# Kernel optimization log

Measured on AMD Instinct MI355X. Metric: run time of the kernel, lower is better.

## Reference

```python
import jax, jax.numpy as jnp
import numpy as np

# Winograd F(4x4, 3x3) transform matrices (wincnn convention, as in jiecaoyu/winograd)
BT = jnp.array([
    [4.,  0., -5.,  0., 1., 0.],
    [0., -4., -4.,  1., 1., 0.],
    [0.,  4., -4., -1., 1., 0.],
    [0., -2., -1.,  2., 1., 0.],
    [0.,  2., -1., -2., 1., 0.],
    [0.,  4.,  0., -5., 0., 1.]], dtype=jnp.float32)  # [6,6]
AT = jnp.array([
    [1., 1.,  1., 1.,  1., 0.],
    [0., 1., -1., 2., -2., 0.],
    [0., 1.,  1., 4.,  4., 0.],
    [0., 1., -1., 8., -8., 1.]], dtype=jnp.float32)  # [4,6]

KERNEL = 3
PAD = 1
GROUPS = 1
TILE_IN = 6   # input_tile_size
TILE_OUT = 4  # output_tile_size


def setup_inputs() -> dict:
    key = jax.random.key(0)
    k1, k2, k3 = jax.random.split(key, 3)
    N, Cin, H, W = 16, 64, 128, 128
    Cout = 64
    x = jax.random.normal(k1, (N, Cin, H, W), dtype=jnp.float32)
    # weight is stored in the Winograd (6x6 spectral) domain, as in the module
    weight = jax.random.normal(k2, (Cout, Cin // GROUPS, TILE_IN, TILE_IN), dtype=jnp.float32) * 0.01
    bias = jax.random.normal(k3, (Cout,), dtype=jnp.float32) * 0.01
    return {"x": x, "weight": weight, "bias": bias}


def reference(x, weight, bias):
    N, Cin, H0, W0 = x.shape
    Cout = weight.shape[0]
    g = GROUPS
    # conv padding
    x = jnp.pad(x, ((0, 0), (0, 0), (PAD, PAD), (PAD, PAD)))
    H = x.shape[2]
    out_w = H - KERNEL + 1
    # pad so output width is a multiple of the output tile size
    extra = (-out_w) % TILE_OUT
    if extra:
        x = jnp.pad(x, ((0, 0), (0, 0), (0, extra), (0, extra)))
    nt = (x.shape[2] - TILE_IN) // TILE_OUT + 1  # tiles per spatial dim
    # extract overlapping 6x6 tiles with stride 4 (the torch unfold)
    idx = jnp.arange(nt)[:, None] * TILE_OUT + jnp.arange(TILE_IN)[None, :]  # [nt,6]
    tiles = x[:, :, idx]                 # [N,C,nt,6,Wp]
    tiles = tiles[:, :, :, :, idx]       # [N,C,nt,6,nt,6]
    # input transform: V = BT @ d @ BT^T per tile -> [N,C,nt,nt,6,6]
    V = jnp.einsum('ai,ncpiqj,bj->ncpqab', BT, tiles, BT)
    # grouped spectral GEMM over input channels
    Vg = V.reshape(N, g, Cin // g, nt, nt, TILE_IN, TILE_IN)
    Wg = weight.reshape(g, Cout // g, Cin // g, TILE_IN, TILE_IN)
    M = jnp.einsum('goiab,ngipqab->ngopqab', Wg, Vg)
    M = M.reshape(N, Cout, nt, nt, TILE_IN, TILE_IN)
    # output transform: Y = AT @ M @ AT^T per tile -> [N,O,nt,nt,4,4]
    Y = jnp.einsum('xa,nopqab,yb->nopqxy', AT, M, AT)
    # stitch tiles back: [N,O,nt,4,nt,4] -> [N,O,nt*4,nt*4]
    y = Y.transpose(0, 1, 2, 4, 3, 5).reshape(N, Cout, nt * TILE_OUT, nt * TILE_OUT)
    y = y + bias[None, :, None, None]
    # crop the extra padding
    y = y[:, :, :out_w, :out_w]
    return y
```

## Files before the change

### kernel.cpp

```cpp
#include <hip/hip_runtime.h>
#include <stdint.h>

typedef __attribute__((ext_vector_type(4))) float f32x4;
typedef __attribute__((ext_vector_type(8))) short s16x8;

#define WB_BYTES 294912

__device__ __forceinline__ short f2bf(float f) {
    uint32_t u = __builtin_bit_cast(uint32_t, f);
    u = u + 0x7FFFu + ((u >> 16) & 1u);
    return (short)(u >> 16);
}

__global__ __launch_bounds__(256) void wtrans(const float* __restrict__ wf, short* __restrict__ wb) {
    int tid = blockIdx.x * 256 + threadIdx.x;
    const float* src = wf + tid * 36;
    float w[36];
#pragma unroll
    for (int i = 0; i < 9; i++) {
        f32x4 v = *(const f32x4*)(src + 4 * i);
        w[4*i+0] = v[0]; w[4*i+1] = v[1]; w[4*i+2] = v[2]; w[4*i+3] = v[3];
    }
#pragma unroll
    for (int ab = 0; ab < 36; ab++) wb[ab * 4096 + tid] = f2bf(w[ab]);
}

#define XS 343
__global__ __launch_bounds__(256, 2) void wino_fused(const float* __restrict__ x,
                                                     const short* __restrict__ wb,
                                                     const float* __restrict__ bias,
                                                     float* __restrict__ out) {
    __shared__ float X[32 * XS];
    __shared__ __align__(16) short Vs[18 * 16 * 32];
    int t = threadIdx.x;
    int lane = t & 63;
    int cog = t >> 6;
    int lo = lane & 15;
    int kq = lane >> 4;

    int b = blockIdx.x;
    int n = b >> 6;
    int sb = b & 63;
    int p0 = (sb >> 3) * 4;
    int q0 = (sb & 7) * 4;
    const float* xb = x + (size_t)n * 64 * 16384;
    int row0 = 4 * p0 - 1;
    int col0a = 4 * q0 - 4;

    int cin = t & 31;
    int tl0 = t >> 5;

    f32x4 acc[36];
#pragma unroll
    for (int i = 0; i < 36; i++) acc[i] = (f32x4){0.f, 0.f, 0.f, 0.f};

#pragma unroll
    for (int r = 0; r < 2; r++) {
#pragma unroll
        for (int i = 0; i < 14; i++) {
            int s = i * 256 + t;
            if (s < 3456) {
                int ci = s / 108;
                int rs = s - ci * 108;
                int row = rs / 6;
                int c4 = rs - row * 6;
                int gr = row0 + row;
                int gc = col0a + 4 * c4;
                float v0 = 0.f, v1 = 0.f, v2 = 0.f, v3 = 0.f;
                if ((unsigned)gr < 128u) {
                    const float* rowp = xb + (size_t)((r * 32 + ci) * 128 + gr) * 128;
                    if (gc >= 0 && gc + 3 < 128) {
                        f32x4 v = *(const f32x4*)(rowp + gc);
                        v0 = v[0]; v1 = v[1]; v2 = v[2]; v3 = v[3];
                    } else {
                        if ((unsigned)(gc + 0) < 128u) v0 = rowp[gc + 0];
                        if ((unsigned)(gc + 1) < 128u) v1 = rowp[gc + 1];
                        if ((unsigned)(gc + 2) < 128u) v2 = rowp[gc + 2];
                        if ((unsigned)(gc + 3) < 128u) v3 = rowp[gc + 3];
                    }
                }
                int base = ci * XS + row * 18;
                int cl = 4 * c4 - 3;
                if ((unsigned)(cl + 0) < 18u) X[base + cl + 0] = v0;
                if ((unsigned)(cl + 1) < 18u) X[base + cl + 1] = v1;
                if ((unsigned)(cl + 2) < 18u) X[base + cl + 2] = v2;
                if ((unsigned)(cl + 3) < 18u) X[base + cl + 3] = v3;
            }
        }
        __syncthreads();

#pragma unroll
        for (int s = 0; s < 2; s++) {
#pragma unroll
            for (int task = 0; task < 2; task++) {
                int tl = tl0 + task * 8;
                int tp = tl >> 2, tq = tl & 3;
                const float* Xb = X + cin * XS + (4 * tp) * 18 + 4 * tq;
                float Ua[3][6];
#pragma unroll
                for (int c = 0; c < 6; c++) {
                    float m0 = Xb[0 * 18 + c], m1 = Xb[1 * 18 + c], m2 = Xb[2 * 18 + c];
                    float m3 = Xb[3 * 18 + c], m4 = Xb[4 * 18 + c], m5 = Xb[5 * 18 + c];
                    if (s == 0) {
                        float e = fmaf(-4.f, m2, m4);
                        float f = fmaf(-4.f, m1, m3);
                        Ua[0][c] = fmaf(4.f, m0 - m2, m4 - m2);
                        Ua[1][c] = e + f;
                        Ua[2][c] = e - f;
                    } else {
                        float g = m4 - m2;
                        float h = m3 - m1;
                        Ua[0][c] = fmaf(2.f, h, g);
                        Ua[1][c] = fmaf(-2.f, h, g);
                        Ua[2][c] = fmaf(4.f, m1 - m3, m5 - m3);
                    }
                }
                short* vb = Vs + tl * 32 + cin;
#pragma unroll
                for (int ar = 0; ar < 3; ar++) {
                    float m0 = Ua[ar][0], m1 = Ua[ar][1], m2 = Ua[ar][2];
                    float m3 = Ua[ar][3], m4 = Ua[ar][4], m5 = Ua[ar][5];
                    float e = fmaf(-4.f, m2, m4);
                    float f = fmaf(-4.f, m1, m3);
                    float g = m4 - m2;
                    float h = m3 - m1;
                    vb[(ar * 6 + 0) * 512] = f2bf(fmaf(4.f, m0 - m2, g));
                    vb[(ar * 6 + 1) * 512] = f2bf(e + f);
                    vb[(ar * 6 + 2) * 512] = f2bf(e - f);
                    vb[(ar * 6 + 3) * 512] = f2bf(fmaf(2.f, h, g));
                    vb[(ar * 6 + 4) * 512] = f2bf(fmaf(-2.f, h, g));
                    vb[(ar * 6 + 5) * 512] = f2bf(fmaf(4.f, m1 - m3, m5 - m3));
                }
            }
            __syncthreads();

            const short* wb_base = wb + (s * 18) * 4096 + (cog * 16 + lo) * 64 + r * 32 + kq * 8;
            const short* v_base = Vs + lo * 32 + kq * 8;
#pragma unroll
            for (int abl = 0; abl < 18; abl++) {
                s16x8 a0 = *(const s16x8*)(wb_base + abl * 4096);
                s16x8 b0 = *(const s16x8*)(v_base + abl * 512);
                acc[s * 18 + abl] = __builtin_amdgcn_mfma_f32_16x16x32_bf16(a0, b0, acc[s * 18 + abl], 0, 0, 0);
            }
            __syncthreads();
        }
    }

    int p = p0 + (lo >> 2);
    int q = q0 + (lo & 3);
#pragma unroll
    for (int rr = 0; rr < 4; rr++) {
        int co = cog * 16 + kq * 4 + rr;
        float bv = bias[co];
        float z[4][6];
#pragma unroll
        for (int bb = 0; bb < 6; bb++) {
            float m0 = acc[0 * 6 + bb][rr], m1 = acc[1 * 6 + bb][rr], m2 = acc[2 * 6 + bb][rr];
            float m3 = acc[3 * 6 + bb][rr], m4 = acc[4 * 6 + bb][rr], m5 = acc[5 * 6 + bb][rr];
            float s1 = m1 + m2, d1 = m1 - m2, s2 = m3 + m4, d2 = m3 - m4;
            z[0][bb] = m0 + s1 + s2;
            z[1][bb] = fmaf(2.f, d2, d1);
            z[2][bb] = fmaf(4.f, s2, s1);
            z[3][bb] = fmaf(8.f, d2, d1) + m5;
        }
        float* ob = out + ((size_t)(n * 64 + co) * 128 + 4 * p) * 128 + 4 * q;
#pragma unroll
        for (int xr = 0; xr < 4; xr++) {
            float s1 = z[xr][1] + z[xr][2], d1 = z[xr][1] - z[xr][2];
            float s2 = z[xr][3] + z[xr][4], d2 = z[xr][3] - z[xr][4];
            f32x4 y;
            y[0] = z[xr][0] + s1 + s2 + bv;
            y[1] = fmaf(2.f, d2, d1) + bv;
            y[2] = fmaf(4.f, s2, s1) + bv;
            y[3] = fmaf(8.f, d2, d1) + z[xr][5] + bv;
            *(f32x4*)(ob + xr * 128) = y;
        }
    }
}

extern "C" void kernel_launch(void* const* d_in, const int* in_sizes, int n_in,
                              void* d_out, int out_size, void* d_ws, size_t ws_size,
                              hipStream_t stream) {
    const float* x    = (const float*)d_in[0];
    const float* wf   = (const float*)d_in[1];
    const float* bias = (const float*)d_in[2];
    float* out = (float*)d_out;

    if (ws_size < WB_BYTES) return;
    short* wb = (short*)d_ws;

    wtrans<<<16, 256, 0, stream>>>(wf, wb);
    wino_fused<<<1024, 256, 0, stream>>>(x, wb, bias, out);
}
```

Baseline: 180.7 us.

## Split output channels across blocks, use direct global-to-LDS loads, stage outputs via LDS

The fused Winograd kernel now splits the 64 output channels into four blocks per spatial tile group, so the grid grows to 4096 blocks and each wave holds 9 accumulators instead of 36. That lowers register pressure and raises the occupancy target to 3 blocks per SIMD. Input tiles are fetched with global_load_lds straight into shared memory, with boundary zeroing done afterwards. Each wave owns 9 of the 36 spectral positions, and the accumulators go through a shared-memory union buffer before the output transform. The cost is that every output-channel block redoes the input load and input transform, adding redundant work and extra global traffic.

```diff
diff --git a/kernel.cpp b/kernel.cpp
--- a/kernel.cpp
+++ b/kernel.cpp
@@ -3,6 +3,8 @@
 
 typedef __attribute__((ext_vector_type(4))) float f32x4;
 typedef __attribute__((ext_vector_type(8))) short s16x8;
+typedef __attribute__((address_space(1))) const char g8_t;
+typedef __attribute__((address_space(3))) char lds8_t;
 
 #define WB_BYTES 294912
 
@@ -25,144 +27,156 @@
     for (int ab = 0; ab < 36; ab++) wb[ab * 4096 + tid] = f2bf(w[ab]);
 }
 
-#define XS 343
-__global__ __launch_bounds__(256, 2) void wino_fused(const float* __restrict__ x,
+__global__ __launch_bounds__(256, 3) void wino_fused(const float* __restrict__ x,
                                                      const short* __restrict__ wb,
                                                      const float* __restrict__ bias,
                                                      float* __restrict__ out) {
-    __shared__ float X[32 * XS];
-    __shared__ __align__(16) short Vs[18 * 16 * 32];
+    __shared__ __align__(16) union UU {
+        struct { float X[16 * 432]; short Vs[36 * 256]; } s;
+        float Mx[36 * 257];
+    } u;
+
     int t = threadIdx.x;
     int lane = t & 63;
-    int cog = t >> 6;
     int lo = lane & 15;
     int kq = lane >> 4;
-
-    int b = blockIdx.x;
-    int n = b >> 6;
-    int sb = b & 63;
-    int p0 = (sb >> 3) * 4;
-    int q0 = (sb & 7) * 4;
+    int wav = t >> 6;
+    int wab0 = wav * 9;
+
+    int bid = blockIdx.x;
+    int g = bid >> 5;
+    int cog = (bid >> 3) & 3;
+    int sb = g * 8 + (bid & 7);
+    int n = sb >> 6;
+    int sb6 = sb & 63;
+    int p0 = (sb6 >> 3) << 2;
+    int q0 = (sb6 & 7) << 2;
     const float* xb = x + (size_t)n * 64 * 16384;
     int row0 = 4 * p0 - 1;
-    int col0a = 4 * q0 - 4;
-
-    int cin = t & 31;
-    int tl0 = t >> 5;
-
-    f32x4 acc[36];
-#pragma unroll
-    for (int i = 0; i < 36; i++) acc[i] = (f32x4){0.f, 0.f, 0.f, 0.f};
-
-#pragma unroll
-    for (int r = 0; r < 2; r++) {
-#pragma unroll
-        for (int i = 0; i < 14; i++) {
-            int s = i * 256 + t;
-            if (s < 3456) {
-                int ci = s / 108;
-                int rs = s - ci * 108;
-                int row = rs / 6;
-                int c4 = rs - row * 6;
+    int col0 = 4 * q0 - 4;
+    bool bnd = (p0 == 0) | (p0 == 28) | (q0 == 0) | (q0 == 28);
+
+    int ci = t & 15;
+    int tile = t >> 4;
+    int ttp = tile >> 2, ttq = tile & 3;
+
+    f32x4 acc[9];
+#pragma unroll
+    for (int i = 0; i < 9; i++) acc[i] = (f32x4){0.f, 0.f, 0.f, 0.f};
+    s16x8 bfrag[9];
+
+    for (int rq = 0; rq < 4; rq++) {
+#pragma unroll
+        for (int i = 0; i < 7; i++) {
+            int k = i * 256 + t;
+            if (k < 1728) {
+                int cc = k / 108;
+                int rem = k - cc * 108;
+                int row = rem / 6;
+                int c4 = rem - row * 6;
                 int gr = row0 + row;
-                int gc = col0a + 4 * c4;
-                float v0 = 0.f, v1 = 0.f, v2 = 0.f, v3 = 0.f;
-                if ((unsigned)gr < 128u) {
-                    const float* rowp = xb + (size_t)((r * 32 + ci) * 128 + gr) * 128;
-                    if (gc >= 0 && gc + 3 < 128) {
-                        f32x4 v = *(const f32x4*)(rowp + gc);
-                        v0 = v[0]; v1 = v[1]; v2 = v[2]; v3 = v[3];
-                    } else {
-                        if ((unsigned)(gc + 0) < 128u) v0 = rowp[gc + 0];
-                        if ((unsigned)(gc + 1) < 128u) v1 = rowp[gc + 1];
-                        if ((unsigned)(gc + 2) < 128u) v2 = rowp[gc + 2];
-                        if ((unsigned)(gc + 3) < 128u) v3 = rowp[gc + 3];
-                    }
-                }
-                int base = ci * XS + row * 18;
-                int cl = 4 * c4 - 3;
-                if ((unsigned)(cl + 0) < 18u) X[base + cl + 0] = v0;
-                if ((unsigned)(cl + 1) < 18u) X[base + cl + 1] = v1;
-                if ((unsigned)(cl + 2) < 18u) X[base + cl + 2] = v2;
-                if ((unsigned)(cl + 3) < 18u) X[base + cl + 3] = v3;
+                int gc = col0 + 4 * c4;
+                bool ok = ((unsigned)gr < 128u) && ((unsigned)gc <= 124u);
+                const float* src = ok ? (xb + ((size_t)((rq * 16 + cc) * 128 + gr)) * 128 + gc) : xb;
+                lds8_t* dst = (lds8_t*)u.s.X + (size_t)(i * 256 + (t & ~63)) * 16;
+                __builtin_amdgcn_global_load_lds((g8_t*)src, dst, 16, 0, 0);
             }
         }
         __syncthreads();
 
-#pragma unroll
-        for (int s = 0; s < 2; s++) {
-#pragma unroll
-            for (int task = 0; task < 2; task++) {
-                int tl = tl0 + task * 8;
-                int tp = tl >> 2, tq = tl & 3;
-                const float* Xb = X + cin * XS + (4 * tp) * 18 + 4 * tq;
-                float Ua[3][6];
-#pragma unroll
-                for (int c = 0; c < 6; c++) {
-                    float m0 = Xb[0 * 18 + c], m1 = Xb[1 * 18 + c], m2 = Xb[2 * 18 + c];
-                    float m3 = Xb[3 * 18 + c], m4 = Xb[4 * 18 + c], m5 = Xb[5 * 18 + c];
-                    if (s == 0) {
-                        float e = fmaf(-4.f, m2, m4);
-                        float f = fmaf(-4.f, m1, m3);
-                        Ua[0][c] = fmaf(4.f, m0 - m2, m4 - m2);
-                        Ua[1][c] = e + f;
-                        Ua[2][c] = e - f;
-                    } else {
-                        float g = m4 - m2;
-                        float h = m3 - m1;
-                        Ua[0][c] = fmaf(2.f, h, g);
-                        Ua[1][c] = fmaf(-2.f, h, g);
-                        Ua[2][c] = fmaf(4.f, m1 - m3, m5 - m3);
-                    }
-                }
-                short* vb = Vs + tl * 32 + cin;
-#pragma unroll
-                for (int ar = 0; ar < 3; ar++) {
-                    float m0 = Ua[ar][0], m1 = Ua[ar][1], m2 = Ua[ar][2];
-                    float m3 = Ua[ar][3], m4 = Ua[ar][4], m5 = Ua[ar][5];
-                    float e = fmaf(-4.f, m2, m4);
-                    float f = fmaf(-4.f, m1, m3);
-                    float g = m4 - m2;
-                    float h = m3 - m1;
-                    vb[(ar * 6 + 0) * 512] = f2bf(fmaf(4.f, m0 - m2, g));
-                    vb[(ar * 6 + 1) * 512] = f2bf(e + f);
-                    vb[(ar * 6 + 2) * 512] = f2bf(e - f);
-                    vb[(ar * 6 + 3) * 512] = f2bf(fmaf(2.f, h, g));
-                    vb[(ar * 6 + 4) * 512] = f2bf(fmaf(-2.f, h, g));
-                    vb[(ar * 6 + 5) * 512] = f2bf(fmaf(4.f, m1 - m3, m5 - m3));
-                }
-            }
+        if (bnd) {
+            if (p0 == 0 && t < 96)  { int c = t / 6, c4 = t - 6 * c;  *(f32x4*)&u.s.X[(c * 108 + 0 * 6 + c4) * 4] = (f32x4){0,0,0,0}; }
+            if (p0 == 28 && t < 96) { int c = t / 6, c4 = t - 6 * c;  *(f32x4*)&u.s.X[(c * 108 + 17 * 6 + c4) * 4] = (f32x4){0,0,0,0}; }
+            if (q0 == 0)  { for (int z = t; z < 288; z += 256) { int c = z / 18, row = z - 18 * c; *(f32x4*)&u.s.X[(c * 108 + row * 6 + 0) * 4] = (f32x4){0,0,0,0}; } }
+            if (q0 == 28) { for (int z = t; z < 288; z += 256) { int c = z / 18, row = z - 18 * c; *(f32x4*)&u.s.X[(c * 108 + row * 6 + 5) * 4] = (f32x4){0,0,0,0}; } }
             __syncthreads();
-
-            const short* wb_base = wb + (s * 18) * 4096 + (cog * 16 + lo) * 64 + r * 32 + kq * 8;
-            const short* v_base = Vs + lo * 32 + kq * 8;
-#pragma unroll
-            for (int abl = 0; abl < 18; abl++) {
-                s16x8 a0 = *(const s16x8*)(wb_base + abl * 4096);
-                s16x8 b0 = *(const s16x8*)(v_base + abl * 512);
-                acc[s * 18 + abl] = __builtin_amdgcn_mfma_f32_16x16x32_bf16(a0, b0, acc[s * 18 + abl], 0, 0, 0);
-            }
-            __syncthreads();
+        }
+
+        {
+            const float* Xr = u.s.X + ci * 432 + (4 * ttp) * 24 + 4 * ttq;
+            float E[6][6];
+#pragma unroll
+            for (int rr = 0; rr < 6; rr++) {
+                f32x4 v0 = *(const f32x4*)(Xr + rr * 24);
+                f32x4 v1 = *(const f32x4*)(Xr + rr * 24 + 4);
+                float v2 = Xr[rr * 24 + 8];
+                float m0 = v0[3], m1 = v1[0], m2 = v1[1], m3 = v1[2], m4 = v1[3], m5 = v2;
+                float e = fmaf(-4.f, m2, m4);
+                float f = fmaf(-4.f, m1, m3);
+                float gg = m4 - m2;
+                float h = m3 - m1;
+                E[rr][0] = fmaf(4.f, m0 - m2, gg);
+                E[rr][1] = e + f;
+                E[rr][2] = e - f;
+                E[rr][3] = fmaf(2.f, h, gg);
+                E[rr][4] = fmaf(-2.f, h, gg);
+                E[rr][5] = fmaf(4.f, m1 - m3, m5 - m3);
+            }
+            short* vbw = u.s.Vs + tile * 16 + ci;
+#pragma unroll
+            for (int b = 0; b < 6; b++) {
+                float m0 = E[0][b], m1 = E[1][b], m2 = E[2][b], m3 = E[3][b], m4 = E[4][b], m5 = E[5][b];
+                float e = fmaf(-4.f, m2, m4);
+                float f = fmaf(-4.f, m1, m3);
+                float gg = m4 - m2;
+                float h = m3 - m1;
+                vbw[(0 * 6 + b) * 256] = f2bf(fmaf(4.f, m0 - m2, gg));
+                vbw[(1 * 6 + b) * 256] = f2bf(e + f);
+                vbw[(2 * 6 + b) * 256] = f2bf(e - f);
+                vbw[(3 * 6 + b) * 256] = f2bf(fmaf(2.f, h, gg));
+                vbw[(4 * 6 + b) * 256] = f2bf(fmaf(-2.f, h, gg));
+                vbw[(5 * 6 + b) * 256] = f2bf(fmaf(4.f, m1 - m3, m5 - m3));
+            }
+        }
+        __syncthreads();
+
+        int qpar = rq & 1;
+        if ((kq >> 1) == qpar) {
+            int koff = (kq & 1) * 8;
+#pragma unroll
+            for (int abl = 0; abl < 9; abl++)
+                bfrag[abl] = *(const s16x8*)(u.s.Vs + (wab0 + abl) * 256 + lo * 16 + koff);
+        }
+        if (qpar) {
+            int half = rq >> 1;
+            const short* wba = wb + (cog * 16 + lo) * 64 + half * 32 + kq * 8;
+#pragma unroll
+            for (int abl = 0; abl < 9; abl++) {
+                s16x8 a = *(const s16x8*)(wba + (wab0 + abl) * 4096);
+                acc[abl] = __builtin_amdgcn_mfma_f32_16x16x32_bf16(a, bfrag[abl], acc[abl], 0, 0, 0);
+            }
         }
     }
-
-    int p = p0 + (lo >> 2);
-    int q = q0 + (lo & 3);
-#pragma unroll
-    for (int rr = 0; rr < 4; rr++) {
-        int co = cog * 16 + kq * 4 + rr;
+    __syncthreads();
+
+#pragma unroll
+    for (int abl = 0; abl < 9; abl++)
+#pragma unroll
+        for (int rr = 0; rr < 4; rr++)
+            u.Mx[(wab0 + abl) * 257 + (kq * 4 + rr) * 16 + lo] = acc[abl][rr];
+    __syncthreads();
+
+    {
+        int c16 = t >> 4;
+        int tl = t & 15;
+        int co = cog * 16 + c16;
         float bv = bias[co];
         float z[4][6];
 #pragma unroll
-        for (int bb = 0; bb < 6; bb++) {
-            float m0 = acc[0 * 6 + bb][rr], m1 = acc[1 * 6 + bb][rr], m2 = acc[2 * 6 + bb][rr];
-            float m3 = acc[3 * 6 + bb][rr], m4 = acc[4 * 6 + bb][rr], m5 = acc[5 * 6 + bb][rr];
+        for (int b = 0; b < 6; b++) {
+            float m0 = u.Mx[(0 * 6 + b) * 257 + c16 * 16 + tl];
+            float m1 = u.Mx[(1 * 6 + b) * 257 + c16 * 16 + tl];
+            float m2 = u.Mx[(2 * 6 + b) * 257 + c16 * 16 + tl];
+            float m3 = u.Mx[(3 * 6 + b) * 257 + c16 * 16 + tl];
+            float m4 = u.Mx[(4 * 6 + b) * 257 + c16 * 16 + tl];
+            float m5 = u.Mx[(5 * 6 + b) * 257 + c16 * 16 + tl];
             float s1 = m1 + m2, d1 = m1 - m2, s2 = m3 + m4, d2 = m3 - m4;
-            z[0][bb] = m0 + s1 + s2;
-            z[1][bb] = fmaf(2.f, d2, d1);
-            z[2][bb] = fmaf(4.f, s2, s1);
-            z[3][bb] = fmaf(8.f, d2, d1) + m5;
-        }
+            z[0][b] = m0 + s1 + s2;
+            z[1][b] = fmaf(2.f, d2, d1);
+            z[2][b] = fmaf(4.f, s2, s1);
+            z[3][b] = fmaf(8.f, d2, d1) + m5;
+        }
+        int p = p0 + (tl >> 2), q = q0 + (tl & 3);
         float* ob = out + ((size_t)(n * 64 + co) * 128 + 4 * p) * 128 + 4 * q;
 #pragma unroll
         for (int xr = 0; xr < 4; xr++) {
@@ -190,5 +204,5 @@
     short* wb = (short*)d_ws;
 
     wtrans<<<16, 256, 0, stream>>>(wf, wb);
-    wino_fused<<<1024, 256, 0, stream>>>(x, wb, bias, out);
-}
+    wino_fused<<<4096, 256, 0, stream>>>(x, wb, bias, out);
+}
```

After: 194.0 us. 7.4% more time.
